# Optimization experiments

Hardware: AMD Instinct MI355X
Metric: run time of the kernel (lower is better)

## Reference

```python
import jax, jax.numpy as jnp
import numpy as np

L = 4        # num_blocks
D = 512      # d_model
H = 8        # num_heads
DFF = 2048   # d_ff
EPS = 1.1920929e-07  # torch RMSNorm default eps = finfo(fp32).eps


def setup_inputs() -> dict:
    key = jax.random.key(0)
    ks = jax.random.split(key, 12)
    B, S = 4, 1024
    s = 0.02
    return {
        "x": jax.random.normal(ks[0], (B, S, D), jnp.float32),
        "col_ids": jax.random.randint(ks[1], (B, S), 0, 32),
        "row_ids": jax.random.randint(ks[2], (B, S), 0, 128),
        "nbr_ids": jax.random.randint(ks[3], (B, S), 0, 64),
        # per-block, per-relation attention weights (nn.Linear: y = x @ W.T)
        "Wq": jax.random.normal(ks[4], (L, 4, D, D), jnp.float32) * s,
        "Wk": jax.random.normal(ks[5], (L, 4, D, D), jnp.float32) * s,
        "Wv": jax.random.normal(ks[6], (L, 4, D, D), jnp.float32) * s,
        "Wo": jax.random.normal(ks[7], (L, 4, D, D), jnp.float32) * s,
        # SwiGLU FFN weights per block
        "W1": jax.random.normal(ks[8], (L, DFF, D), jnp.float32) * s,
        "W3": jax.random.normal(ks[9], (L, DFF, D), jnp.float32) * s,
        "W2": jax.random.normal(ks[10], (L, D, DFF), jnp.float32) * s,
        # RMSNorm scales: 4 attn norms + 1 ffn norm per block + final norm_out
        "g_attn": jnp.ones((L, 4, D), jnp.float32),
        "g_ffn": jnp.ones((L, D), jnp.float32),
        "g_out": jnp.ones((D,), jnp.float32),
    }


def _rms(x, g):
    return x * jax.lax.rsqrt(jnp.mean(x * x, axis=-1, keepdims=True) + EPS) * g


def _attn(x, wq, wk, wv, wo, mask):
    # x: [B,S,D]; mask: [B,S,S] bool (True = attend) or None for full attention
    B, S, _ = x.shape
    hd = D // H
    scale = 1.0 / np.sqrt(hd).astype(np.float32)
    q = (x @ wq.T).reshape(B, S, H, hd).transpose(0, 2, 1, 3)  # bhsd
    k = (x @ wk.T).reshape(B, S, H, hd).transpose(0, 2, 1, 3)
    v = (x @ wv.T).reshape(B, S, H, hd).transpose(0, 2, 1, 3)
    sc = jnp.einsum('bhqd,bhkd->bhqk', q, k) * scale
    if mask is not None:
        sc = jnp.where(mask[:, None, :, :], sc, jnp.float32(-1e30))
    a = jax.nn.softmax(sc, axis=-1)
    o = jnp.einsum('bhqk,bhkd->bhqd', a, v).transpose(0, 2, 1, 3).reshape(B, S, D)
    return o @ wo.T


def reference(x, col_ids, row_ids, nbr_ids, Wq, Wk, Wv, Wo, W1, W3, W2, g_attn, g_ffn, g_out):
    # relation order in RelationalBlock: col, feat, nbr, full
    masks = [ids[:, :, None] == ids[:, None, :] for ids in (col_ids, row_ids, nbr_ids)] + [None]
    for l in range(L):
        for r in range(4):
            x = x + _attn(_rms(x, g_attn[l, r]), Wq[l, r], Wk[l, r], Wv[l, r], Wo[l, r], masks[r])
        h = _rms(x, g_ffn[l])
        x = x + (jax.nn.silu(h @ W1[l].T) * (h @ W3[l].T)) @ W2[l].T
    return _rms(x, g_out)
```

## Files before the change

kernel.cpp:

```cpp
#include <hip/hip_runtime.h>
#include <hip/hip_bf16.h>


typedef __attribute__((ext_vector_type(4))) float f32x4;
typedef __attribute__((ext_vector_type(8))) short s16x8;
typedef __attribute__((ext_vector_type(4))) short s16x4;

#define SEQ 1024
#define DM 512
#define MTOT 4096
#define EPSV 1.1920929e-07f
#define LOG2E 1.44269504088896f

static __device__ __forceinline__ float b2f(short s) {
  unsigned u = ((unsigned)(unsigned short)s) << 16;
  return __builtin_bit_cast(float, u);
}
static __device__ __forceinline__ short f2b(float f) {
  unsigned u = __builtin_bit_cast(unsigned, f);
  u = (u + 0x7fffu + ((u >> 16) & 1u)) >> 16;
  return (short)(unsigned short)u;
}

#define MFMA_BF16(a, b, c) __builtin_amdgcn_mfma_f32_16x16x32_bf16((a), (b), (c), 0, 0, 0)
#define GLLDS(gp, lp)                                                                        \
  __builtin_amdgcn_global_load_lds((const __attribute__((address_space(1))) unsigned*)(gp),  \
                                   (__attribute__((address_space(3))) unsigned*)(lp), 16, 0, 0)
#define GLLDS4(gp, lp)                                                                       \
  __builtin_amdgcn_global_load_lds((const __attribute__((address_space(1))) unsigned*)(gp),  \
                                   (__attribute__((address_space(3))) unsigned*)(lp), 4, 0, 0)

__global__ void cvt_all(const f32x4* __restrict__ wq, const f32x4* __restrict__ wk,
                        const f32x4* __restrict__ wv, const f32x4* __restrict__ wo,
                        const f32x4* __restrict__ w1, const f32x4* __restrict__ w3,
                        const f32x4* __restrict__ w2, const float* __restrict__ g_attn,
                        const float* __restrict__ g_ffn, s16x4* __restrict__ wqkv,
                        s16x4* __restrict__ wob, s16x4* __restrict__ w13,
                        s16x4* __restrict__ w2b) {
  int i = blockIdx.x * 256 + threadIdx.x;
  int which = blockIdx.y;
  s16x4 o;
  if (which < 3) {
    const f32x4* src = which == 0 ? wq : (which == 1 ? wk : wv);
    f32x4 v = src[i];
    int lr = i >> 16, k4 = i & 127, n = (i >> 7) & 511;
    const float* gp = g_attn + lr * 512 + k4 * 4;
    float sc = (which == 0) ? 0.125f * LOG2E : 1.0f;
#pragma unroll
    for (int j = 0; j < 4; j++) o[j] = f2b(v[j] * gp[j] * sc);
    wqkv[(size_t)lr * 196608 + (which * 512 + n) * 128 + k4] = o;
  } else if (which == 3) {
    f32x4 v = wo[i];
#pragma unroll
    for (int j = 0; j < 4; j++) o[j] = f2b(v[j]);
    wob[i] = o;
  } else if (which < 6) {
    const f32x4* src = which == 4 ? w1 : w3;
    int off = which - 4;
    f32x4 v = src[i];
    int l = i >> 18, n = (i >> 7) & 2047, k4 = i & 127;
    const float* gp = g_ffn + l * 512 + k4 * 4;
#pragma unroll
    for (int j = 0; j < 4; j++) o[j] = f2b(v[j] * gp[j]);
    w13[(size_t)l * 524288 + (n * 2 + off) * 128 + k4] = o;
  } else {
    f32x4 v = w2[i];
#pragma unroll
    for (int j = 0; j < 4; j++) o[j] = f2b(v[j]);
    w2b[i] = o;
  }
}

__global__ void init_kernel(const float* __restrict__ xin, float* __restrict__ x,
                            short* __restrict__ h, float* __restrict__ ssq) {
  int row = blockIdx.x * 4 + (threadIdx.x >> 6);
  int lane = threadIdx.x & 63;
  const float* xr = xin + (size_t)row * DM + lane * 8;
  f32x4 a = *(const f32x4*)xr;
  f32x4 b = *(const f32x4*)(xr + 4);
  float* xo = x + (size_t)row * DM + lane * 8;
  *(f32x4*)xo = a;
  *(f32x4*)(xo + 4) = b;
  s16x8 ho;
#pragma unroll
  for (int j = 0; j < 4; j++) { ho[j] = f2b(a[j]); ho[4 + j] = f2b(b[j]); }
  *(s16x8*)(h + (size_t)row * DM + lane * 8) = ho;
  float ss = a[0]*a[0]+a[1]*a[1]+a[2]*a[2]+a[3]*a[3]+b[0]*b[0]+b[1]*b[1]+b[2]*b[2]+b[3]*b[3];
#pragma unroll
  for (int m = 1; m < 64; m <<= 1) ss += __shfl_xor(ss, m, 64);
  if (lane == 0) ssq[row] = ss;
}

__global__ void rmsnorm_out(const float* __restrict__ x, const float* __restrict__ g,
                            float* __restrict__ outp) {
  int row = blockIdx.x * 4 + (threadIdx.x >> 6);
  int lane = threadIdx.x & 63;
  const float* xr = x + (size_t)row * DM + lane * 8;
  f32x4 a = *(const f32x4*)xr;
  f32x4 b = *(const f32x4*)(xr + 4);
  float ss = a[0]*a[0]+a[1]*a[1]+a[2]*a[2]+a[3]*a[3]+b[0]*b[0]+b[1]*b[1]+b[2]*b[2]+b[3]*b[3];
#pragma unroll
  for (int m = 1; m < 64; m <<= 1) ss += __shfl_xor(ss, m, 64);
  float sc = rsqrtf(ss * (1.0f / DM) + EPSV);
  const float* gp = g + lane * 8;
  float* o = outp + (size_t)row * DM + lane * 8;
  f32x4 o0, o1;
#pragma unroll
  for (int j = 0; j < 4; j++) { o0[j] = a[j] * sc * gp[j]; o1[j] = b[j] * sc * gp[4 + j]; }
  *(f32x4*)o = o0;
  *(f32x4*)(o + 4) = o1;
}

template<int AR, int AC, int FUSE>
__global__ __launch_bounds__(256) void gemm_bt(const short* __restrict__ A, const short* __restrict__ W,
                                               short* __restrict__ outb, float* __restrict__ outf,
                                               short* __restrict__ vtb,
                                               const float* __restrict__ ssq_in,
                                               float* __restrict__ ssq_out,
                                               short* __restrict__ hb, int N, int K) {
  constexpr int BM = AR * 32;
  constexpr int BN = AC * 32;
  constexpr int NA = BM / 64, NB = BN / 64;
  constexpr int LPS = NA + NB;
  __shared__ short As[2][BM * 32];
  __shared__ short Bs[2][BN * 32];
  const int tid = threadIdx.x;
  const int lane = tid & 63;
  const int w = tid >> 6;
  const int wr = w >> 1, wc = w & 1;
  const int qi = lane & 15, g = lane >> 4;
  const int m0 = blockIdx.x * BM, n0 = blockIdx.y * BN;

  const short* ap[NA];
  const short* wp[NB];
#pragma unroll
  for (int i = 0; i < NA; i++) {
    int s = i * 256 + tid;
    int row = s >> 2, gl = s & 3, gd = gl ^ ((row >> 1) & 3);
    ap[i] = A + (size_t)(m0 + row) * K + gd * 8;
  }
#pragma unroll
  for (int i = 0; i < NB; i++) {
    int s = i * 256 + tid;
    int row = s >> 2, gl = s & 3, gd = gl ^ ((row >> 1) & 3);
    wp[i] = W + (size_t)(n0 + row) * K + gd * 8;
  }
  int aro[AR], bro[AC];
#pragma unroll
  for (int i = 0; i < AR; i++) {
    int row = wr * AR * 16 + i * 16 + qi;
    aro[i] = row * 64 + ((g ^ ((row >> 1) & 3)) * 16);
  }
#pragma unroll
  for (int j = 0; j < AC; j++) {
    int row = wc * AC * 16 + j * 16 + qi;
    bro[j] = row * 64 + ((g ^ ((row >> 1) & 3)) * 16);
  }
  f32x4 acc[AR][AC] = {};

#define STAGE_G(BUF)                                                             \
  {                                                                              \
    _Pragma("unroll")                                                            \
    for (int i = 0; i < NA; i++) {                                               \
      GLLDS(ap[i], (char*)As[BUF] + (i * 256 + w * 64) * 16);                    \
      ap[i] += 32;                                                               \
    }                                                                            \
    _Pragma("unroll")                                                            \
    for (int i = 0; i < NB; i++) {                                               \
      GLLDS(wp[i], (char*)Bs[BUF] + (i * 256 + w * 64) * 16);                    \
      wp[i] += 32;                                                               \
    }                                                                            \
  }

#define BODY_G(BUF, T)                                                           \
  {                                                                              \
    s16x8 af[AR], bf[AC];                                                        \
    _Pragma("unroll")                                                            \
    for (int i = 0; i < AR; i++) af[i] = *(const s16x8*)((char*)As[BUF] + aro[i]); \
    _Pragma("unroll")                                                            \
    for (int j = 0; j < AC; j++) bf[j] = *(const s16x8*)((char*)Bs[BUF] + bro[j]); \
    asm volatile("s_waitcnt lgkmcnt(0)" ::: "memory");                           \
    __builtin_amdgcn_s_barrier();                                                \
    bool more = ((T) + 2 < nt);                                                  \
    if (more) STAGE_G(BUF);                                                      \
    _Pragma("unroll")                                                            \
    for (int i = 0; i < AR; i++)                                                 \
      _Pragma("unroll")                                                          \
      for (int j = 0; j < AC; j++)                                               \
        acc[i][j] = MFMA_BF16(af[i], bf[j], acc[i][j]);                          \
    if (more) asm volatile("s_waitcnt vmcnt(%0)" :: "n"(LPS) : "memory");        \
    else      asm volatile("s_waitcnt vmcnt(0)" ::: "memory");                   \
    __builtin_amdgcn_s_barrier();                                                \
  }

  const int nt = K >> 5;
  STAGE_G(0);
  STAGE_G(1);
  asm volatile("s_waitcnt vmcnt(%0)" :: "n"(LPS) : "memory");
  __builtin_amdgcn_s_barrier();
  for (int t = 0; t < nt; t += 2) {
    BODY_G(0, t);
    BODY_G(1, t + 1);
  }
#undef STAGE_G
#undef BODY_G

  float srow[AR][4];
  if (FUSE == 2 || FUSE == 3) {
#pragma unroll
    for (int i = 0; i < AR; i++) {
      int rbase = m0 + wr * AR * 16 + i * 16 + g * 4;
#pragma unroll
      for (int r = 0; r < 4; r++)
        srow[i][r] = rsqrtf(ssq_in[rbase + r] * (1.0f / DM) + EPSV);
    }
  }
  float part[AR][4];
  if (FUSE == 1) {
#pragma unroll
    for (int i = 0; i < AR; i++)
#pragma unroll
      for (int r = 0; r < 4; r++) part[i][r] = 0.f;
  }

#pragma unroll
  for (int i = 0; i < AR; i++) {
    int rbase = m0 + wr * AR * 16 + i * 16 + g * 4;
#pragma unroll
    for (int j = 0; j < AC; j++) {
      int col = n0 + wc * AC * 16 + j * 16 + qi;
      if (FUSE == 2 && col >= 1024) {
        int bbv = rbase >> 10, s = rbase & 1023;
        int c = col - 1024, hhv = c >> 6, d = c & 63;
        int o = (s & 63) >> 2;
        int gg = o & 3, h2 = (o >> 2) & 1, q32 = o >> 3;
        int pnew = q32 * 8 + gg * 2 + h2;
        s16x4 o4;
#pragma unroll
        for (int r = 0; r < 4; r++) o4[r] = f2b(acc[i][j][r] * srow[i][r]);
        *(s16x4*)(vtb + (((size_t)(bbv * 8 + hhv) * 64 + d) << 10) + (s & ~63) + pnew * 4) = o4;
      } else if (FUSE == 3) {
#pragma unroll
        for (int r = 0; r < 4; r++) {
          float own = acc[i][j][r] * srow[i][r];
          float other = __shfl_xor(own, 1, 64);
          float sv = own / (1.0f + __expf(-own));
          if (!(lane & 1))
            outb[(size_t)(rbase + r) * (N >> 1) + (col >> 1)] = f2b(sv * other);
        }
      } else if (FUSE == 1) {
#pragma unroll
        for (int r = 0; r < 4; r++) {
          size_t idx = (size_t)(rbase + r) * N + col;
          float xnew = outf[idx] + acc[i][j][r];
          outf[idx] = xnew;
          hb[idx] = f2b(xnew);
          part[i][r] += xnew * xnew;
        }
      } else {
#pragma unroll
        for (int r = 0; r < 4; r++)
          outb[(size_t)(rbase + r) * N + col] = f2b(acc[i][j][r] * srow[i][r]);
      }
    }
  }
  if (FUSE == 1) {
#pragma unroll
    for (int i = 0; i < AR; i++) {
      int rbase = m0 + wr * AR * 16 + i * 16 + g * 4;
#pragma unroll
      for (int r = 0; r < 4; r++) {
        float p = part[i][r];
#pragma unroll
        for (int m = 1; m < 16; m <<= 1) p += __shfl_xor(p, m, 16);
        if (qi == 0) atomicAdd(&ssq_out[rbase + r], p);
      }
    }
  }
}

__global__ __launch_bounds__(256) void attn_kernel(const short* __restrict__ qkv, const short* __restrict__ vt,
                                                   const int* __restrict__ ids, short* __restrict__ Ob) {
  const int bh = blockIdx.x;
  const int bb = bh >> 3, hh = bh & 7;
  const int q0 = blockIdx.y * 64;
  const int tid = threadIdx.x, lane = tid & 63, w = tid >> 6;
  const int g = lane >> 4, qi = lane & 15;
  __shared__ short Kl[2][128 * 64];
  __shared__ short Vl[2][64 * 128];
  __shared__ int Kid[2][128];
  const short* kbase = qkv + 512 + hh * 64;
  const short* vbase = vt + (size_t)bh * 64 * SEQ;
  s16x8 qf0, qf1;
  {
    int qrow = q0 + w * 16 + qi;
    const short* qp = qkv + (size_t)(bb * SEQ + qrow) * 1536 + hh * 64 + g * 8;
    qf0 = *(const s16x8*)qp;
    qf1 = *(const s16x8*)(qp + 32);
  }
  int qid = 0;
  if (ids) qid = ids[bb * SEQ + q0 + w * 16 + qi];
  float m_ = -1e30f, l_ = 0.f;
  f32x4 oacc[4] = {};

#define STAGE_ATTN(buf, ktt)                                                                     \
  {                                                                                              \
    _Pragma("unroll")                                                                            \
    for (int i = 0; i < 4; i++) {                                                                \
      int s = i * 256 + tid;                                                                     \
      int row = s >> 3, gl = s & 7, gd = gl ^ (row & 7);                                         \
      GLLDS(kbase + (size_t)(bb * SEQ + (ktt) + row) * 1536 + gd * 8,                            \
            (char*)Kl[buf] + (i * 256 + w * 64) * 16);                                           \
    }                                                                                            \
    _Pragma("unroll")                                                                            \
    for (int i = 0; i < 4; i++) {                                                                \
      int s = i * 256 + tid;                                                                     \
      int d = s >> 4, gl = s & 15, gd = gl ^ (d & 7);                                            \
      GLLDS(vbase + (size_t)d * SEQ + (ktt) + gd * 8, (char*)Vl[buf] + (i * 256 + w * 64) * 16); \
    }                                                                                            \
    if (ids && w < 2) GLLDS4(ids + bb * SEQ + (ktt) + w * 64 + lane, (char*)Kid[buf] + w * 256); \
  }

  STAGE_ATTN(0, 0);
  __syncthreads();
  int cur = 0;
  for (int kt = 0; kt < SEQ; kt += 128) {
    if (kt + 128 < SEQ) STAGE_ATTN(cur ^ 1, kt + 128);
    f32x4 sc[8];
#pragma unroll
    for (int kc = 0; kc < 8; kc++) {
      int krow = kc * 16 + qi;
      s16x8 kf0 = *(const s16x8*)(Kl[cur] + krow * 64 + ((g ^ (krow & 7)) * 8));
      s16x8 kf1 = *(const s16x8*)(Kl[cur] + krow * 64 + (((4 + g) ^ (krow & 7)) * 8));
      f32x4 s4 = {};
      s4 = MFMA_BF16(kf0, qf0, s4);
      s4 = MFMA_BF16(kf1, qf1, s4);
      sc[kc] = s4;
    }
    float p[8][4];
#pragma unroll
    for (int kc = 0; kc < 8; kc++)
#pragma unroll
      for (int r = 0; r < 4; r++) p[kc][r] = sc[kc][r];
    if (ids) {
#pragma unroll
      for (int kc = 0; kc < 8; kc++) {
        int4 kid4 = *(const int4*)(Kid[cur] + kc * 16 + g * 4);
        if (kid4.x != qid) p[kc][0] = -1e30f;
        if (kid4.y != qid) p[kc][1] = -1e30f;
        if (kid4.z != qid) p[kc][2] = -1e30f;
        if (kid4.w != qid) p[kc][3] = -1e30f;
      }
    }
    float mx = fmaxf(fmaxf(p[0][0], p[0][1]), fmaxf(p[0][2], p[0][3]));
#pragma unroll
    for (int kc = 1; kc < 8; kc++)
      mx = fmaxf(mx, fmaxf(fmaxf(p[kc][0], p[kc][1]), fmaxf(p[kc][2], p[kc][3])));
    mx = fmaxf(mx, __shfl_xor(mx, 16, 64));
    mx = fmaxf(mx, __shfl_xor(mx, 32, 64));
    if (__any(mx > m_ + 8.f)) {
      float nm = fmaxf(m_, mx);
      float c = exp2f(m_ - nm);
      m_ = nm;
      l_ *= c;
#pragma unroll
      for (int r = 0; r < 4; r++) {
        float cr = __shfl(c, g * 4 + r, 16);
        oacc[0][r] *= cr; oacc[1][r] *= cr; oacc[2][r] *= cr; oacc[3][r] *= cr;
      }
    }
    float sum = 0.f;
#pragma unroll
    for (int kc = 0; kc < 8; kc++)
#pragma unroll
      for (int r = 0; r < 4; r++) {
        p[kc][r] = exp2f(p[kc][r] - m_);
        sum += p[kc][r];
      }
    sum += __shfl_xor(sum, 16, 64);
    sum += __shfl_xor(sum, 32, 64);
    l_ += sum;
#pragma unroll
    for (int kk = 0; kk < 2; kk++) {
      s16x8 pa, pb;
#pragma unroll
      for (int r = 0; r < 4; r++) {
        pa[r] = f2b(p[kk * 4 + 0][r]); pa[4 + r] = f2b(p[kk * 4 + 1][r]);
        pb[r] = f2b(p[kk * 4 + 2][r]); pb[4 + r] = f2b(p[kk * 4 + 3][r]);
      }
#pragma unroll
      for (int dt = 0; dt < 4; dt++) {
        int dl = dt * 16 + qi;
        const short* vr = Vl[cur] + dl * 128;
        s16x8 vf0 = *(const s16x8*)(vr + (kk * 8 + (g ^ (dl & 7))) * 8);
        s16x8 vf1 = *(const s16x8*)(vr + (kk * 8 + ((4 + g) ^ (dl & 7))) * 8);
        oacc[dt] = MFMA_BF16(pa, vf0, oacc[dt]);
        oacc[dt] = MFMA_BF16(pb, vf1, oacc[dt]);
      }
    }
    __syncthreads();
    cur ^= 1;
  }
#undef STAGE_ATTN
  const size_t obase = (size_t)(bb * SEQ) * DM + hh * 64;
#pragma unroll
  for (int r = 0; r < 4; r++) {
    float lr = __shfl(l_, g * 4 + r, 16);
    float inv = 1.0f / lr;
    int q = q0 + w * 16 + g * 4 + r;
#pragma unroll
    for (int dt = 0; dt < 4; dt++)
      Ob[obase + (size_t)q * DM + dt * 16 + qi] = f2b(oacc[dt][r] * inv);
  }
}

extern "C" void kernel_launch(void* const* d_in, const int* in_sizes, int n_in,
                              void* d_out, int out_size, void* d_ws, size_t ws_size,
                              hipStream_t stream) {
  const float* x_in  = (const float*)d_in[0];
  const int* col_ids = (const int*)d_in[1];
  const int* row_ids = (const int*)d_in[2];
  const int* nbr_ids = (const int*)d_in[3];
  const float* g_attn = (const float*)d_in[11];
  const float* g_ffn  = (const float*)d_in[12];
  const float* g_out  = (const float*)d_in[13];

  char* ws = (char*)d_ws;
  float* x    = (float*)(ws);
  short* h    = (short*)(ws + (size_t)(8u  << 20));
  short* qkv  = (short*)(ws + (size_t)(12u << 20));
  short* vt   = (short*)(ws + (size_t)(24u << 20));
  short* ob   = (short*)(ws + (size_t)(28u << 20));
  float* sbuf = (float*)(ws + (size_t)(33u << 20));
  short* fa   = (short*)(ws + (size_t)(44u << 20));
  short* wqkv = (short*)(ws + (size_t)(60u  << 20));
  short* wob  = (short*)(ws + (size_t)(84u  << 20));
  short* w13  = (short*)(ws + (size_t)(92u  << 20));
  short* w2b  = (short*)(ws + (size_t)(108u << 20));

  hipMemsetAsync(sbuf, 0, 21 * 4096 * sizeof(float), stream);
  cvt_all<<<dim3(4096, 7), 256, 0, stream>>>((const f32x4*)d_in[4], (const f32x4*)d_in[5],
                                             (const f32x4*)d_in[6], (const f32x4*)d_in[7],
                                             (const f32x4*)d_in[8], (const f32x4*)d_in[9],
                                             (const f32x4*)d_in[10], g_attn, g_ffn,
                                             (s16x4*)wqkv, (s16x4*)wob, (s16x4*)w13, (s16x4*)w2b);
  init_kernel<<<1024, 256, 0, stream>>>(x_in, x, h, sbuf);

  const int* idsarr[4] = {col_ids, row_ids, nbr_ids, nullptr};

  for (int l = 0; l < 4; l++) {
    for (int r = 0; r < 4; r++) {
      int slot = l * 5 + r;
      size_t woff = (size_t)(l * 4 + r) * 1536 * DM;
      gemm_bt<4, 2, 2><<<dim3(32, 24), 256, 0, stream>>>(h, wqkv + woff, qkv, nullptr, vt,
                                                         sbuf + (size_t)slot * 4096, nullptr,
                                                         nullptr, 1536, DM);
      attn_kernel<<<dim3(32, 16), 256, 0, stream>>>(qkv, vt, idsarr[r], ob);
      gemm_bt<2, 2, 1><<<dim3(64, 8), 256, 0, stream>>>(ob, wob + (size_t)(l * 4 + r) * DM * DM,
                                                        nullptr, x, nullptr, nullptr,
                                                        sbuf + (size_t)(slot + 1) * 4096, h, DM, DM);
    }
    int fslot = l * 5 + 4;
    gemm_bt<4, 2, 3><<<dim3(32, 64), 256, 0, stream>>>(h, w13 + (size_t)l * 4096 * DM, fa, nullptr,
                                                       nullptr, sbuf + (size_t)fslot * 4096,
                                                       nullptr, nullptr, 4096, DM);
    gemm_bt<2, 2, 1><<<dim3(64, 8), 256, 0, stream>>>(fa, w2b + (size_t)l * DM * 2048, nullptr, x,
                                                      nullptr, nullptr,
                                                      sbuf + (size_t)(fslot + 1) * 4096, h, DM, 2048);
  }
  rmsnorm_out<<<1024, 256, 0, stream>>>(x, g_out, (float*)d_out);
}
```

Before: 1.134 ms.

## Shrink attention tiles for more blocks, widen weight conversion, fold memset into init

```diff
diff --git a/kernel.cpp b/kernel.cpp
--- a/kernel.cpp
+++ b/kernel.cpp
@@ -5,6 +5,7 @@
 typedef __attribute__((ext_vector_type(4))) float f32x4;
 typedef __attribute__((ext_vector_type(8))) short s16x8;
 typedef __attribute__((ext_vector_type(4))) short s16x4;
+typedef __attribute__((ext_vector_type(16))) short s16x16;
 
 #define SEQ 1024
 #define DM 512
@@ -34,45 +35,56 @@
                         const f32x4* __restrict__ wv, const f32x4* __restrict__ wo,
                         const f32x4* __restrict__ w1, const f32x4* __restrict__ w3,
                         const f32x4* __restrict__ w2, const float* __restrict__ g_attn,
-                        const float* __restrict__ g_ffn, s16x4* __restrict__ wqkv,
-                        s16x4* __restrict__ wob, s16x4* __restrict__ w13,
-                        s16x4* __restrict__ w2b) {
-  int i = blockIdx.x * 256 + threadIdx.x;
+                        const float* __restrict__ g_ffn, short* __restrict__ wqkv,
+                        short* __restrict__ wob, short* __restrict__ w13,
+                        short* __restrict__ w2b) {
+  int i0 = (blockIdx.x * 256 + threadIdx.x) * 4;
   int which = blockIdx.y;
-  s16x4 o;
+  s16x16 o;
   if (which < 3) {
     const f32x4* src = which == 0 ? wq : (which == 1 ? wk : wv);
-    f32x4 v = src[i];
-    int lr = i >> 16, k4 = i & 127, n = (i >> 7) & 511;
+    f32x4 v[4];
+#pragma unroll
+    for (int c = 0; c < 4; c++) v[c] = src[i0 + c];
+    int lr = i0 >> 16, k4 = i0 & 127, n = (i0 >> 7) & 511;
     const float* gp = g_attn + lr * 512 + k4 * 4;
     float sc = (which == 0) ? 0.125f * LOG2E : 1.0f;
 #pragma unroll
-    for (int j = 0; j < 4; j++) o[j] = f2b(v[j] * gp[j] * sc);
-    wqkv[(size_t)lr * 196608 + (which * 512 + n) * 128 + k4] = o;
-  } else if (which == 3) {
-    f32x4 v = wo[i];
-#pragma unroll
-    for (int j = 0; j < 4; j++) o[j] = f2b(v[j]);
-    wob[i] = o;
-  } else if (which < 6) {
+    for (int c = 0; c < 4; c++)
+#pragma unroll
+      for (int j = 0; j < 4; j++) o[c * 4 + j] = f2b(v[c][j] * gp[c * 4 + j] * sc);
+    *(s16x16*)(wqkv + ((size_t)lr * 196608 + (which * 512 + n) * 128 + k4) * 4) = o;
+  } else if (which == 3 || which == 6) {
+    const f32x4* src = which == 3 ? wo : w2;
+    short* dst = which == 3 ? wob : w2b;
+    f32x4 v[4];
+#pragma unroll
+    for (int c = 0; c < 4; c++) v[c] = src[i0 + c];
+#pragma unroll
+    for (int c = 0; c < 4; c++)
+#pragma unroll
+      for (int j = 0; j < 4; j++) o[c * 4 + j] = f2b(v[c][j]);
+    *(s16x16*)(dst + (size_t)i0 * 4) = o;
+  } else {
     const f32x4* src = which == 4 ? w1 : w3;
     int off = which - 4;
-    f32x4 v = src[i];
-    int l = i >> 18, n = (i >> 7) & 2047, k4 = i & 127;
+    f32x4 v[4];
+#pragma unroll
+    for (int c = 0; c < 4; c++) v[c] = src[i0 + c];
+    int l = i0 >> 18, n = (i0 >> 7) & 2047, k4 = i0 & 127;
     const float* gp = g_ffn + l * 512 + k4 * 4;
 #pragma unroll
-    for (int j = 0; j < 4; j++) o[j] = f2b(v[j] * gp[j]);
-    w13[(size_t)l * 524288 + (n * 2 + off) * 128 + k4] = o;
-  } else {
-    f32x4 v = w2[i];
-#pragma unroll
-    for (int j = 0; j < 4; j++) o[j] = f2b(v[j]);
-    w2b[i] = o;
+    for (int c = 0; c < 4; c++)
+#pragma unroll
+      for (int j = 0; j < 4; j++) o[c * 4 + j] = f2b(v[c][j] * gp[c * 4 + j]);
+    *(s16x16*)(w13 + ((size_t)l * 524288 + (n * 2 + off) * 128 + k4) * 4) = o;
   }
 }
 
 __global__ void init_kernel(const float* __restrict__ xin, float* __restrict__ x,
-                            short* __restrict__ h, float* __restrict__ ssq) {
+                            short* __restrict__ h, float* __restrict__ sbuf) {
+  int gid = blockIdx.x * 256 + threadIdx.x;
+  if (gid < 20 * 4096) sbuf[4096 + gid] = 0.f;
   int row = blockIdx.x * 4 + (threadIdx.x >> 6);
   int lane = threadIdx.x & 63;
   const float* xr = xin + (size_t)row * DM + lane * 8;
@@ -88,7 +100,7 @@
   float ss = a[0]*a[0]+a[1]*a[1]+a[2]*a[2]+a[3]*a[3]+b[0]*b[0]+b[1]*b[1]+b[2]*b[2]+b[3]*b[3];
 #pragma unroll
   for (int m = 1; m < 64; m <<= 1) ss += __shfl_xor(ss, m, 64);
-  if (lane == 0) ssq[row] = ss;
+  if (lane == 0) sbuf[row] = ss;
 }
 
 __global__ void rmsnorm_out(const float* __restrict__ x, const float* __restrict__ g,
@@ -279,16 +291,16 @@
   }
 }
 
-__global__ __launch_bounds__(256) void attn_kernel(const short* __restrict__ qkv, const short* __restrict__ vt,
+__global__ __launch_bounds__(128) void attn_kernel(const short* __restrict__ qkv, const short* __restrict__ vt,
                                                    const int* __restrict__ ids, short* __restrict__ Ob) {
   const int bh = blockIdx.x;
   const int bb = bh >> 3, hh = bh & 7;
-  const int q0 = blockIdx.y * 64;
+  const int q0 = blockIdx.y * 32;
   const int tid = threadIdx.x, lane = tid & 63, w = tid >> 6;
   const int g = lane >> 4, qi = lane & 15;
-  __shared__ short Kl[2][128 * 64];
-  __shared__ short Vl[2][64 * 128];
-  __shared__ int Kid[2][128];
+  __shared__ short Kl[2][64 * 64];
+  __shared__ short Vl[2][64 * 64];
+  __shared__ int Kid[2][64];
   const short* kbase = qkv + 512 + hh * 64;
   const short* vbase = vt + (size_t)bh * 64 * SEQ;
   s16x8 qf0, qf1;
@@ -307,28 +319,28 @@
   {                                                                                              \
     _Pragma("unroll")                                                                            \
     for (int i = 0; i < 4; i++) {                                                                \
-      int s = i * 256 + tid;                                                                     \
+      int s = i * 128 + tid;                                                                     \
       int row = s >> 3, gl = s & 7, gd = gl ^ (row & 7);                                         \
       GLLDS(kbase + (size_t)(bb * SEQ + (ktt) + row) * 1536 + gd * 8,                            \
-            (char*)Kl[buf] + (i * 256 + w * 64) * 16);                                           \
+            (char*)Kl[buf] + (i * 128 + w * 64) * 16);                                           \
     }                                                                                            \
     _Pragma("unroll")                                                                            \
     for (int i = 0; i < 4; i++) {                                                                \
-      int s = i * 256 + tid;                                                                     \
-      int d = s >> 4, gl = s & 15, gd = gl ^ (d & 7);                                            \
-      GLLDS(vbase + (size_t)d * SEQ + (ktt) + gd * 8, (char*)Vl[buf] + (i * 256 + w * 64) * 16); \
+      int s = i * 128 + tid;                                                                     \
+      int d = s >> 3, gl = s & 7, gd = gl ^ (d & 7);                                             \
+      GLLDS(vbase + (size_t)d * SEQ + (ktt) + gd * 8, (char*)Vl[buf] + (i * 128 + w * 64) * 16); \
     }                                                                                            \
-    if (ids && w < 2) GLLDS4(ids + bb * SEQ + (ktt) + w * 64 + lane, (char*)Kid[buf] + w * 256); \
+    if (ids && w == 0) GLLDS4(ids + bb * SEQ + (ktt) + lane, (char*)Kid[buf]);                   \
   }
 
   STAGE_ATTN(0, 0);
   __syncthreads();
   int cur = 0;
-  for (int kt = 0; kt < SEQ; kt += 128) {
-    if (kt + 128 < SEQ) STAGE_ATTN(cur ^ 1, kt + 128);
-    f32x4 sc[8];
-#pragma unroll
-    for (int kc = 0; kc < 8; kc++) {
+  for (int kt = 0; kt < SEQ; kt += 64) {
+    if (kt + 64 < SEQ) STAGE_ATTN(cur ^ 1, kt + 64);
+    f32x4 sc[4];
+#pragma unroll
+    for (int kc = 0; kc < 4; kc++) {
       int krow = kc * 16 + qi;
       s16x8 kf0 = *(const s16x8*)(Kl[cur] + krow * 64 + ((g ^ (krow & 7)) * 8));
       s16x8 kf1 = *(const s16x8*)(Kl[cur] + krow * 64 + (((4 + g) ^ (krow & 7)) * 8));
@@ -337,14 +349,14 @@
       s4 = MFMA_BF16(kf1, qf1, s4);
       sc[kc] = s4;
     }
-    float p[8][4];
-#pragma unroll
-    for (int kc = 0; kc < 8; kc++)
+    float p[4][4];
+#pragma unroll
+    for (int kc = 0; kc < 4; kc++)
 #pragma unroll
       for (int r = 0; r < 4; r++) p[kc][r] = sc[kc][r];
     if (ids) {
 #pragma unroll
-      for (int kc = 0; kc < 8; kc++) {
+      for (int kc = 0; kc < 4; kc++) {
         int4 kid4 = *(const int4*)(Kid[cur] + kc * 16 + g * 4);
         if (kid4.x != qid) p[kc][0] = -1e30f;
         if (kid4.y != qid) p[kc][1] = -1e30f;
@@ -354,7 +366,7 @@
     }
     float mx = fmaxf(fmaxf(p[0][0], p[0][1]), fmaxf(p[0][2], p[0][3]));
 #pragma unroll
-    for (int kc = 1; kc < 8; kc++)
+    for (int kc = 1; kc < 4; kc++)
       mx = fmaxf(mx, fmaxf(fmaxf(p[kc][0], p[kc][1]), fmaxf(p[kc][2], p[kc][3])));
     mx = fmaxf(mx, __shfl_xor(mx, 16, 64));
     mx = fmaxf(mx, __shfl_xor(mx, 32, 64));
@@ -371,7 +383,7 @@
     }
     float sum = 0.f;
 #pragma unroll
-    for (int kc = 0; kc < 8; kc++)
+    for (int kc = 0; kc < 4; kc++)
 #pragma unroll
       for (int r = 0; r < 4; r++) {
         p[kc][r] = exp2f(p[kc][r] - m_);
@@ -380,23 +392,20 @@
     sum += __shfl_xor(sum, 16, 64);
     sum += __shfl_xor(sum, 32, 64);
     l_ += sum;
-#pragma unroll
-    for (int kk = 0; kk < 2; kk++) {
-      s16x8 pa, pb;
-#pragma unroll
-      for (int r = 0; r < 4; r++) {
-        pa[r] = f2b(p[kk * 4 + 0][r]); pa[4 + r] = f2b(p[kk * 4 + 1][r]);
-        pb[r] = f2b(p[kk * 4 + 2][r]); pb[4 + r] = f2b(p[kk * 4 + 3][r]);
-      }
-#pragma unroll
-      for (int dt = 0; dt < 4; dt++) {
-        int dl = dt * 16 + qi;
-        const short* vr = Vl[cur] + dl * 128;
-        s16x8 vf0 = *(const s16x8*)(vr + (kk * 8 + (g ^ (dl & 7))) * 8);
-        s16x8 vf1 = *(const s16x8*)(vr + (kk * 8 + ((4 + g) ^ (dl & 7))) * 8);
-        oacc[dt] = MFMA_BF16(pa, vf0, oacc[dt]);
-        oacc[dt] = MFMA_BF16(pb, vf1, oacc[dt]);
-      }
+    s16x8 pa, pb;
+#pragma unroll
+    for (int r = 0; r < 4; r++) {
+      pa[r] = f2b(p[0][r]); pa[4 + r] = f2b(p[1][r]);
+      pb[r] = f2b(p[2][r]); pb[4 + r] = f2b(p[3][r]);
+    }
+#pragma unroll
+    for (int dt = 0; dt < 4; dt++) {
+      int dl = dt * 16 + qi;
+      const short* vr = Vl[cur] + dl * 64;
+      s16x8 vf0 = *(const s16x8*)(vr + ((g ^ (dl & 7)) * 8));
+      s16x8 vf1 = *(const s16x8*)(vr + (((4 + g) ^ (dl & 7)) * 8));
+      oacc[dt] = MFMA_BF16(pa, vf0, oacc[dt]);
+      oacc[dt] = MFMA_BF16(pb, vf1, oacc[dt]);
     }
     __syncthreads();
     cur ^= 1;
@@ -438,12 +447,11 @@
   short* w13  = (short*)(ws + (size_t)(92u  << 20));
   short* w2b  = (short*)(ws + (size_t)(108u << 20));
 
-  hipMemsetAsync(sbuf, 0, 21 * 4096 * sizeof(float), stream);
-  cvt_all<<<dim3(4096, 7), 256, 0, stream>>>((const f32x4*)d_in[4], (const f32x4*)d_in[5],
+  cvt_all<<<dim3(1024, 7), 256, 0, stream>>>((const f32x4*)d_in[4], (const f32x4*)d_in[5],
                                              (const f32x4*)d_in[6], (const f32x4*)d_in[7],
                                              (const f32x4*)d_in[8], (const f32x4*)d_in[9],
                                              (const f32x4*)d_in[10], g_attn, g_ffn,
-                                             (s16x4*)wqkv, (s16x4*)wob, (s16x4*)w13, (s16x4*)w2b);
+                                             wqkv, wob, w13, w2b);
   init_kernel<<<1024, 256, 0, stream>>>(x_in, x, h, sbuf);
 
   const int* idsarr[4] = {col_ids, row_ids, nbr_ids, nullptr};
@@ -455,7 +463,7 @@
       gemm_bt<4, 2, 2><<<dim3(32, 24), 256, 0, stream>>>(h, wqkv + woff, qkv, nullptr, vt,
                                                          sbuf + (size_t)slot * 4096, nullptr,
                                                          nullptr, 1536, DM);
-      attn_kernel<<<dim3(32, 16), 256, 0, stream>>>(qkv, vt, idsarr[r], ob);
+      attn_kernel<<<dim3(32, 32), 128, 0, stream>>>(qkv, vt, idsarr[r], ob);
       gemm_bt<2, 2, 1><<<dim3(64, 8), 256, 0, stream>>>(ob, wob + (size_t)(l * 4 + r) * DM * DM,
                                                         nullptr, x, nullptr, nullptr,
                                                         sbuf + (size_t)(slot + 1) * 4096, h, DM, DM);
```

New measurement: 1.214 ms. 7.0% more time.
